# Kernel optimization log

Hardware: AMD Instinct MI355X
Metric: run time of the kernel (lower is better)

Reference implementation:

```python
import jax, jax.numpy as jnp
import numpy as np

B, S, D, V = 256, 128, 768, 30522
MASK_ID = 103
# vocab ids of the label words (8 positive, 6 neutral, 7 negative)
LABEL_IDS = [
    [2307, 2204, 3835, 2157, 6581, 2986, 5151, 3893],
    [7929, 24791, 8699, 4257, 16021, 6623],
    [6659, 2919, 11771, 3532, 11325, 4997, 13135],
]


def setup_inputs() -> dict:
    key = jax.random.key(0)
    ks = jax.random.split(key, 12)
    length = jax.random.randint(ks[0], (B,), 5, 105)          # 3+length <= 108 < S
    input_ids = jax.random.randint(ks[1], (B, S), 200, 30000)  # never hits MASK_ID
    input_ids = input_ids.at[jnp.arange(B), 3 + length].set(MASK_ID)  # one [MASK] per row
    bert_out = jax.random.normal(ks[2], (B, S, D), dtype=jnp.float32)
    p = lambda k, shp: 0.02 * jax.random.normal(k, shp, dtype=jnp.float32)
    return {
        'bert_out': bert_out,
        'input_ids': input_ids,
        'length': length,
        'senti_w': p(ks[3], (2, D)), 'senti_b': p(ks[4], (2,)),
        'dense_w': p(ks[5], (D, 2 * D)), 'dense_b': p(ks[6], (D,)),
        'dec_w': p(ks[7], (V, D)), 'dec_b': p(ks[8], (V,)),
        'w0': p(ks[9], (2, 8)), 'w1': p(ks[10], (2, 6)), 'w2': p(ks[11], (2, 7)),
    }


def reference(bert_out, input_ids, length, senti_w, senti_b, dense_w, dense_b,
              dec_w, dec_b, w0, w1, w2):
    # pooler -> sentiment head (Dropout is identity at inference)
    pooler = bert_out[:, 0]                                   # [B, D]
    category_out = pooler @ senti_w.T + senti_b               # [B, 2]

    # per-row [MASK] hidden state (exactly one MASK_ID per row)
    mask_pos = jnp.argmax(input_ids == MASK_ID, axis=1)       # [B]
    mask_logits = jnp.take_along_axis(bert_out, mask_pos[:, None, None], axis=1)[:, 0]  # [B, D]

    # attention(): softmax over the ragged slice bert_out[i, 3:3+length[i]]
    scores_raw = jnp.einsum('bsd,bd->bs', bert_out, mask_logits)        # [B, S]
    idx = jnp.arange(S)
    valid = (idx[None, :] >= 3) & (idx[None, :] < 3 + length[:, None])  # [B, S]
    scores = jax.nn.softmax(jnp.where(valid, scores_raw, -jnp.inf), axis=1)
    scores = jnp.where(valid, scores, 0.0)
    att = jnp.einsum('bs,bsd->bd', scores, bert_out)          # [B, D]

    feats = jnp.concatenate([att, mask_logits], axis=1)       # [B, 2D]
    h = jnp.tanh(feats @ dense_w.T + dense_b)                 # [B, D]
    probs = jnp.tanh(h @ dec_w.T + dec_b)                     # [B, V]

    outs = []
    for ids, w in zip(LABEL_IDS, (w0, w1, w2)):
        lp = probs[:, jnp.array(ids)]                         # [B, k]
        outs.append(lp @ w.T)                                 # [B, 2]
    out = jnp.stack(outs, axis=2)                             # [B, 2, 3]
    return category_out, out
```

## Files before the change

kernel.cpp:

```cpp
#include <hip/hip_runtime.h>
#include <hip/hip_bf16.h>
#include <math.h>

#define BB 256
#define SS 128
#define DD 768
#define K2 1536
#define MASK_ID 103

typedef __attribute__((ext_vector_type(8))) short short8;
typedef __attribute__((ext_vector_type(4))) float floatx4;

__constant__ int c_ids[21] = {
    2307, 2204, 3835, 2157, 6581, 2986, 5151, 3893,
    7929, 24791, 8699, 4257, 16021, 6623,
    6659, 2919, 11771, 3532, 11325, 4997, 13135
};

__device__ __forceinline__ float waveReduceSum(float v) {
    #pragma unroll
    for (int off = 32; off > 0; off >>= 1) v += __shfl_down(v, off, 64);
    return v;
}
__device__ __forceinline__ unsigned short f2bf(float f) {
    unsigned int u = __float_as_uint(f);
    u += 0x7FFF + ((u >> 16) & 1);
    return (unsigned short)(u >> 16);
}

__global__ __launch_bounds__(1024) void k_att(
    const float* __restrict__ bert, const int* __restrict__ ids,
    const int* __restrict__ len, const float* __restrict__ senti_w,
    const float* __restrict__ senti_b, float* __restrict__ cat_out,
    unsigned short* __restrict__ feats,
    const float* __restrict__ dense_w, unsigned short* __restrict__ dwb)
{
    __shared__ __align__(16) float s_mask[DD];
    __shared__ __align__(16) float s_part[16][DD];
    __shared__ float s_m[16], s_l[16], s_scale[16];
    __shared__ float s_red[32];
    __shared__ float s_M;
    __shared__ int s_mp;

    const int b = blockIdx.x;
    const int tid = threadIdx.x;
    const int lane = tid & 63;
    const int wave = tid >> 6;

    if (tid == 0) s_mp = SS;

    {
        const int n4 = DD * K2 / 4;
        for (int i = b * 1024 + tid; i < n4; i += BB * 1024) {
            float4 v = ((const float4*)dense_w)[i];
            ushort4 o;
            o.x = f2bf(v.x); o.y = f2bf(v.y); o.z = f2bf(v.z); o.w = f2bf(v.w);
            ((ushort4*)dwb)[i] = o;
        }
    }

    __syncthreads();
    if (tid < SS && ids[b * SS + tid] == MASK_ID) atomicMin(&s_mp, tid);
    __syncthreads();
    const int mp = (s_mp == SS) ? 0 : s_mp;
    const int L = len[b];
    const float* base = bert + (size_t)b * SS * DD;
    const float* mrow = base + (size_t)mp * DD;

    float c0 = 0.f, c1 = 0.f;
    if (tid < DD) {
        s_mask[tid] = mrow[tid];
        float x = base[tid];
        c0 = x * senti_w[tid];
        c1 = x * senti_w[DD + tid];
    }
    c0 = waveReduceSum(c0);
    c1 = waveReduceSum(c1);
    if (lane == 0) { s_red[wave] = c0; s_red[16 + wave] = c1; }
    __syncthreads();
    if (tid == 0) {
        float t0 = 0.f, t1 = 0.f;
        #pragma unroll
        for (int w = 0; w < 16; ++w) { t0 += s_red[w]; t1 += s_red[16 + w]; }
        cat_out[b * 2 + 0] = t0 + senti_b[0];
        cat_out[b * 2 + 1] = t1 + senti_b[1];
    }

    const float4* m4 = (const float4*)s_mask;
    float4 mm0 = m4[lane], mm1 = m4[lane + 64], mm2 = m4[lane + 128];
    float4 A0 = {0,0,0,0}, A1 = {0,0,0,0}, A2 = {0,0,0,0};
    float mloc = -INFINITY, lloc = 0.f;
    const int end = 3 + L;
    int s = 3 + wave;
    for (; s + 48 < end; s += 64) {
        const float4* r0 = (const float4*)(base + (size_t)s * DD);
        const float4* r1 = (const float4*)(base + (size_t)(s + 16) * DD);
        const float4* r2 = (const float4*)(base + (size_t)(s + 32) * DD);
        const float4* r3 = (const float4*)(base + (size_t)(s + 48) * DD);
        float4 a0 = r0[lane], a1 = r0[lane + 64], a2 = r0[lane + 128];
        float4 b0 = r1[lane], b1 = r1[lane + 64], b2 = r1[lane + 128];
        float4 c0v = r2[lane], c1v = r2[lane + 64], c2v = r2[lane + 128];
        float4 e0 = r3[lane], e1 = r3[lane + 64], e2 = r3[lane + 128];
        float d1 = a0.x*mm0.x + a0.y*mm0.y + a0.z*mm0.z + a0.w*mm0.w
                 + a1.x*mm1.x + a1.y*mm1.y + a1.z*mm1.z + a1.w*mm1.w
                 + a2.x*mm2.x + a2.y*mm2.y + a2.z*mm2.z + a2.w*mm2.w;
        float d2 = b0.x*mm0.x + b0.y*mm0.y + b0.z*mm0.z + b0.w*mm0.w
                 + b1.x*mm1.x + b1.y*mm1.y + b1.z*mm1.z + b1.w*mm1.w
                 + b2.x*mm2.x + b2.y*mm2.y + b2.z*mm2.z + b2.w*mm2.w;
        float d3 = c0v.x*mm0.x + c0v.y*mm0.y + c0v.z*mm0.z + c0v.w*mm0.w
                 + c1v.x*mm1.x + c1v.y*mm1.y + c1v.z*mm1.z + c1v.w*mm1.w
                 + c2v.x*mm2.x + c2v.y*mm2.y + c2v.z*mm2.z + c2v.w*mm2.w;
        float d4 = e0.x*mm0.x + e0.y*mm0.y + e0.z*mm0.z + e0.w*mm0.w
                 + e1.x*mm1.x + e1.y*mm1.y + e1.z*mm1.z + e1.w*mm1.w
                 + e2.x*mm2.x + e2.y*mm2.y + e2.z*mm2.z + e2.w*mm2.w;
        #pragma unroll
        for (int off = 32; off > 0; off >>= 1) {
            d1 += __shfl_xor(d1, off, 64);
            d2 += __shfl_xor(d2, off, 64);
            d3 += __shfl_xor(d3, off, 64);
            d4 += __shfl_xor(d4, off, 64);
        }
        float mnew = fmaxf(fmaxf(fmaxf(d1, d2), fmaxf(d3, d4)), mloc);
        float scale = __expf(mloc - mnew);
        float p1 = __expf(d1 - mnew);
        float p2 = __expf(d2 - mnew);
        float p3 = __expf(d3 - mnew);
        float p4 = __expf(d4 - mnew);
        lloc = lloc * scale + p1 + p2 + p3 + p4;
        A0.x = A0.x*scale + p1*a0.x + p2*b0.x + p3*c0v.x + p4*e0.x;
        A0.y = A0.y*scale + p1*a0.y + p2*b0.y + p3*c0v.y + p4*e0.y;
        A0.z = A0.z*scale + p1*a0.z + p2*b0.z + p3*c0v.z + p4*e0.z;
        A0.w = A0.w*scale + p1*a0.w + p2*b0.w + p3*c0v.w + p4*e0.w;
        A1.x = A1.x*scale + p1*a1.x + p2*b1.x + p3*c1v.x + p4*e1.x;
        A1.y = A1.y*scale + p1*a1.y + p2*b1.y + p3*c1v.y + p4*e1.y;
        A1.z = A1.z*scale + p1*a1.z + p2*b1.z + p3*c1v.z + p4*e1.z;
        A1.w = A1.w*scale + p1*a1.w + p2*b1.w + p3*c1v.w + p4*e1.w;
        A2.x = A2.x*scale + p1*a2.x + p2*b2.x + p3*c2v.x + p4*e2.x;
        A2.y = A2.y*scale + p1*a2.y + p2*b2.y + p3*c2v.y + p4*e2.y;
        A2.z = A2.z*scale + p1*a2.z + p2*b2.z + p3*c2v.z + p4*e2.z;
        A2.w = A2.w*scale + p1*a2.w + p2*b2.w + p3*c2v.w + p4*e2.w;
        mloc = mnew;
    }
    for (; s + 16 < end; s += 32) {
        const float4* ra = (const float4*)(base + (size_t)s * DD);
        const float4* rb = (const float4*)(base + (size_t)(s + 16) * DD);
        float4 a0 = ra[lane], a1 = ra[lane + 64], a2 = ra[lane + 128];
        float4 b0 = rb[lane], b1 = rb[lane + 64], b2 = rb[lane + 128];
        float d1 = a0.x*mm0.x + a0.y*mm0.y + a0.z*mm0.z + a0.w*mm0.w
                 + a1.x*mm1.x + a1.y*mm1.y + a1.z*mm1.z + a1.w*mm1.w
                 + a2.x*mm2.x + a2.y*mm2.y + a2.z*mm2.z + a2.w*mm2.w;
        float d2 = b0.x*mm0.x + b0.y*mm0.y + b0.z*mm0.z + b0.w*mm0.w
                 + b1.x*mm1.x + b1.y*mm1.y + b1.z*mm1.z + b1.w*mm1.w
                 + b2.x*mm2.x + b2.y*mm2.y + b2.z*mm2.z + b2.w*mm2.w;
        #pragma unroll
        for (int off = 32; off > 0; off >>= 1) {
            d1 += __shfl_xor(d1, off, 64);
            d2 += __shfl_xor(d2, off, 64);
        }
        float mnew = fmaxf(mloc, fmaxf(d1, d2));
        float scale = __expf(mloc - mnew);
        float p1 = __expf(d1 - mnew);
        float p2 = __expf(d2 - mnew);
        lloc = lloc * scale + p1 + p2;
        A0.x = A0.x*scale + p1*a0.x + p2*b0.x; A0.y = A0.y*scale + p1*a0.y + p2*b0.y;
        A0.z = A0.z*scale + p1*a0.z + p2*b0.z; A0.w = A0.w*scale + p1*a0.w + p2*b0.w;
        A1.x = A1.x*scale + p1*a1.x + p2*b1.x; A1.y = A1.y*scale + p1*a1.y + p2*b1.y;
        A1.z = A1.z*scale + p1*a1.z + p2*b1.z; A1.w = A1.w*scale + p1*a1.w + p2*b1.w;
        A2.x = A2.x*scale + p1*a2.x + p2*b2.x; A2.y = A2.y*scale + p1*a2.y + p2*b2.y;
        A2.z = A2.z*scale + p1*a2.z + p2*b2.z; A2.w = A2.w*scale + p1*a2.w + p2*b2.w;
        mloc = mnew;
    }
    for (; s < end; s += 16) {
        const float4* ra = (const float4*)(base + (size_t)s * DD);
        float4 a0 = ra[lane], a1 = ra[lane + 64], a2 = ra[lane + 128];
        float d1 = a0.x*mm0.x + a0.y*mm0.y + a0.z*mm0.z + a0.w*mm0.w
                 + a1.x*mm1.x + a1.y*mm1.y + a1.z*mm1.z + a1.w*mm1.w
                 + a2.x*mm2.x + a2.y*mm2.y + a2.z*mm2.z + a2.w*mm2.w;
        #pragma unroll
        for (int off = 32; off > 0; off >>= 1) d1 += __shfl_xor(d1, off, 64);
        float mnew = fmaxf(mloc, d1);
        float scale = __expf(mloc - mnew);
        float p1 = __expf(d1 - mnew);
        lloc = lloc * scale + p1;
        A0.x = A0.x*scale + p1*a0.x; A0.y = A0.y*scale + p1*a0.y;
        A0.z = A0.z*scale + p1*a0.z; A0.w = A0.w*scale + p1*a0.w;
        A1.x = A1.x*scale + p1*a1.x; A1.y = A1.y*scale + p1*a1.y;
        A1.z = A1.z*scale + p1*a1.z; A1.w = A1.w*scale + p1*a1.w;
        A2.x = A2.x*scale + p1*a2.x; A2.y = A2.y*scale + p1*a2.y;
        A2.z = A2.z*scale + p1*a2.z; A2.w = A2.w*scale + p1*a2.w;
        mloc = mnew;
    }
    if (lane == 0) { s_m[wave] = mloc; s_l[wave] = lloc; }
    float4* pw = (float4*)s_part[wave];
    pw[lane] = A0; pw[lane + 64] = A1; pw[lane + 128] = A2;
    __syncthreads();

    if (tid == 0) {
        float M = -INFINITY;
        #pragma unroll
        for (int w = 0; w < 16; ++w) M = fmaxf(M, s_m[w]);
        s_M = M;
    }
    __syncthreads();
    if (tid < 16) s_scale[tid] = __expf(s_m[tid] - s_M);
    __syncthreads();

    if (tid < DD) {
        float lt = 0.f, a = 0.f;
        #pragma unroll
        for (int w = 0; w < 16; ++w) {
            lt += s_scale[w] * s_l[w];
            a  += s_scale[w] * s_part[w][tid];
        }
        unsigned short* fb = feats + (size_t)b * K2;
        fb[tid]      = f2bf(a / lt);
        fb[DD + tid] = f2bf(s_mask[tid]);
    }
}

__global__ __launch_bounds__(512) void k_dense(
    const unsigned short* __restrict__ featsb,
    const unsigned short* __restrict__ dwb,
    const float* __restrict__ db, float* __restrict__ h)
{
    __shared__ floatx4 s_acc[4][64];
    const int tid = threadIdx.x;
    const int lane = tid & 63, wave = tid >> 6;
    const int wq = wave & 3, kh = wave >> 2;
    const int b0 = blockIdx.y * 32 + (wq >> 1) * 16;
    const int j0 = blockIdx.x * 32 + (wq & 1) * 16;
    const int m = lane & 15, q = lane >> 4;

    const short8* Arow = (const short8*)(featsb + (size_t)(b0 + m) * K2) + kh * 96;
    const short8* Brow = (const short8*)(dwb + (size_t)(j0 + m) * K2) + kh * 96;
    floatx4 acc = {0.f, 0.f, 0.f, 0.f};
    #pragma unroll 6
    for (int k8 = 0; k8 < 96; k8 += 4) {
        short8 a = Arow[k8 + q];
        short8 w = Brow[k8 + q];
        acc = __builtin_amdgcn_mfma_f32_16x16x32_bf16(a, w, acc, 0, 0, 0);
    }
    if (kh) s_acc[wq][lane] = acc;
    __syncthreads();
    if (!kh) {
        floatx4 o = s_acc[wq][lane];
        acc.x += o.x; acc.y += o.y; acc.z += o.z; acc.w += o.w;
        const int col = j0 + m;
        const int rb = b0 + q * 4;
        const float bias = db[col];
        #pragma unroll
        for (int r = 0; r < 4; ++r)
            h[(size_t)(rb + r) * DD + col] = tanhf(acc[r] + bias);
    }
}

__global__ __launch_bounds__(256) void k_dec(
    const float* __restrict__ h, const float* __restrict__ dec_w,
    const float* __restrict__ dec_b, const float* __restrict__ w0,
    const float* __restrict__ w1, const float* __restrict__ w2,
    float* __restrict__ out)
{
    __shared__ __align__(16) float s_h[DD];
    __shared__ float s_p[21];
    const int b = blockIdx.x;
    const int tid = threadIdx.x;
    const int lane = tid & 63, wave = tid >> 6;

    for (int d = tid; d < DD; d += 256) s_h[d] = h[(size_t)b * DD + d];
    __syncthreads();

    const float4* h4 = (const float4*)s_h;
    float4 x0 = h4[lane], x1 = h4[lane + 64], x2 = h4[lane + 128];

    for (int idx = wave; idx < 21; idx += 4) {
        const int vid = c_ids[idx];
        const float4* wr = (const float4*)(dec_w + (size_t)vid * DD);
        float4 v0 = wr[lane], v1 = wr[lane + 64], v2 = wr[lane + 128];
        float acc = x0.x*v0.x + x0.y*v0.y + x0.z*v0.z + x0.w*v0.w
                  + x1.x*v1.x + x1.y*v1.y + x1.z*v1.z + x1.w*v1.w
                  + x2.x*v2.x + x2.y*v2.y + x2.z*v2.z + x2.w*v2.w;
        acc = waveReduceSum(acc);
        if (lane == 0) s_p[idx] = tanhf(acc + dec_b[vid]);
    }
    __syncthreads();

    if (tid < 6) {
        const int c = tid / 3, g = tid % 3;
        const float* wg = (g == 0) ? w0 : (g == 1) ? w1 : w2;
        const int n    = (g == 0) ? 8  : (g == 1) ? 6  : 7;
        const int base = (g == 0) ? 0  : (g == 1) ? 8  : 14;
        float acc = 0.f;
        for (int i = 0; i < n; ++i) acc += s_p[base + i] * wg[c * n + i];
        out[(size_t)b * 6 + c * 3 + g] = acc;
    }
}

extern "C" void kernel_launch(void* const* d_in, const int* in_sizes, int n_in,
                              void* d_out, int out_size, void* d_ws, size_t ws_size,
                              hipStream_t stream) {
    const float* bert    = (const float*)d_in[0];
    const int*   ids     = (const int*)  d_in[1];
    const int*   len     = (const int*)  d_in[2];
    const float* senti_w = (const float*)d_in[3];
    const float* senti_b = (const float*)d_in[4];
    const float* dense_w = (const float*)d_in[5];
    const float* dense_b = (const float*)d_in[6];
    const float* dec_w   = (const float*)d_in[7];
    const float* dec_b   = (const float*)d_in[8];
    const float* w0      = (const float*)d_in[9];
    const float* w1      = (const float*)d_in[10];
    const float* w2      = (const float*)d_in[11];
    float* out = (float*)d_out;

    unsigned short* feats = (unsigned short*)d_ws;
    unsigned short* dwb   = feats + (size_t)BB * K2;
    float* h = (float*)(dwb + (size_t)DD * K2);

    k_att<<<BB, 1024, 0, stream>>>(bert, ids, len, senti_w, senti_b, out,
                                   feats, dense_w, dwb);
    k_dense<<<dim3(24, 8), 512, 0, stream>>>(feats, dwb, dense_b, h);
    k_dec<<<BB, 256, 0, stream>>>(h, dec_w, dec_b, w0, w1, w2, out + BB * 2);
}
```

Measured before the change: 221.4 us.

## Fuse dense projection and label-word decoder into one kernel via shared memory

Merges the dense bf16 MFMA GEMM and the label-word decoder/projection into a single kernel. Each 1024-thread block handles 16 batch rows and keeps the tanh hidden states in LDS instead of writing them to global memory. This removes one kernel launch and the global round trip of h. In exchange, the GEMM runs on only 16 blocks with longer per-wave K loops, which reduces parallelism across the GPU.

```diff
diff --git a/kernel.cpp b/kernel.cpp
--- a/kernel.cpp
+++ b/kernel.cpp
@@ -218,80 +218,72 @@
     }
 }
 
-__global__ __launch_bounds__(512) void k_dense(
+#define HP 772
+__global__ __launch_bounds__(1024) void k_dd(
     const unsigned short* __restrict__ featsb,
     const unsigned short* __restrict__ dwb,
-    const float* __restrict__ db, float* __restrict__ h)
+    const float* __restrict__ db,
+    const float* __restrict__ dec_w, const float* __restrict__ dec_b,
+    const float* __restrict__ w0, const float* __restrict__ w1,
+    const float* __restrict__ w2, float* __restrict__ out)
 {
-    __shared__ floatx4 s_acc[4][64];
+    __shared__ __align__(16) float s_h[16][HP];
+    __shared__ float s_p[16][21];
     const int tid = threadIdx.x;
     const int lane = tid & 63, wave = tid >> 6;
-    const int wq = wave & 3, kh = wave >> 2;
-    const int b0 = blockIdx.y * 32 + (wq >> 1) * 16;
-    const int j0 = blockIdx.x * 32 + (wq & 1) * 16;
+    const int b0 = blockIdx.x * 16;
     const int m = lane & 15, q = lane >> 4;
 
-    const short8* Arow = (const short8*)(featsb + (size_t)(b0 + m) * K2) + kh * 96;
-    const short8* Brow = (const short8*)(dwb + (size_t)(j0 + m) * K2) + kh * 96;
-    floatx4 acc = {0.f, 0.f, 0.f, 0.f};
-    #pragma unroll 6
-    for (int k8 = 0; k8 < 96; k8 += 4) {
+    const int j0 = wave * 48;
+    const short8* Arow = (const short8*)(featsb + (size_t)(b0 + m) * K2);
+    const short8* B0 = (const short8*)(dwb + (size_t)(j0      + m) * K2);
+    const short8* B1 = (const short8*)(dwb + (size_t)(j0 + 16 + m) * K2);
+    const short8* B2 = (const short8*)(dwb + (size_t)(j0 + 32 + m) * K2);
+    floatx4 ac0 = {0,0,0,0}, ac1 = {0,0,0,0}, ac2 = {0,0,0,0};
+    #pragma unroll 2
+    for (int k8 = 0; k8 < 192; k8 += 4) {
         short8 a = Arow[k8 + q];
-        short8 w = Brow[k8 + q];
-        acc = __builtin_amdgcn_mfma_f32_16x16x32_bf16(a, w, acc, 0, 0, 0);
-    }
-    if (kh) s_acc[wq][lane] = acc;
-    __syncthreads();
-    if (!kh) {
-        floatx4 o = s_acc[wq][lane];
-        acc.x += o.x; acc.y += o.y; acc.z += o.z; acc.w += o.w;
-        const int col = j0 + m;
-        const int rb = b0 + q * 4;
-        const float bias = db[col];
-        #pragma unroll
-        for (int r = 0; r < 4; ++r)
-            h[(size_t)(rb + r) * DD + col] = tanhf(acc[r] + bias);
-    }
-}
-
-__global__ __launch_bounds__(256) void k_dec(
-    const float* __restrict__ h, const float* __restrict__ dec_w,
-    const float* __restrict__ dec_b, const float* __restrict__ w0,
-    const float* __restrict__ w1, const float* __restrict__ w2,
-    float* __restrict__ out)
-{
-    __shared__ __align__(16) float s_h[DD];
-    __shared__ float s_p[21];
-    const int b = blockIdx.x;
-    const int tid = threadIdx.x;
-    const int lane = tid & 63, wave = tid >> 6;
-
-    for (int d = tid; d < DD; d += 256) s_h[d] = h[(size_t)b * DD + d];
-    __syncthreads();
-
-    const float4* h4 = (const float4*)s_h;
-    float4 x0 = h4[lane], x1 = h4[lane + 64], x2 = h4[lane + 128];
-
-    for (int idx = wave; idx < 21; idx += 4) {
-        const int vid = c_ids[idx];
-        const float4* wr = (const float4*)(dec_w + (size_t)vid * DD);
-        float4 v0 = wr[lane], v1 = wr[lane + 64], v2 = wr[lane + 128];
-        float acc = x0.x*v0.x + x0.y*v0.y + x0.z*v0.z + x0.w*v0.w
-                  + x1.x*v1.x + x1.y*v1.y + x1.z*v1.z + x1.w*v1.w
-                  + x2.x*v2.x + x2.y*v2.y + x2.z*v2.z + x2.w*v2.w;
-        acc = waveReduceSum(acc);
-        if (lane == 0) s_p[idx] = tanhf(acc + dec_b[vid]);
-    }
-    __syncthreads();
-
-    if (tid < 6) {
-        const int c = tid / 3, g = tid % 3;
+        ac0 = __builtin_amdgcn_mfma_f32_16x16x32_bf16(a, B0[k8 + q], ac0, 0, 0, 0);
+        ac1 = __builtin_amdgcn_mfma_f32_16x16x32_bf16(a, B1[k8 + q], ac1, 0, 0, 0);
+        ac2 = __builtin_amdgcn_mfma_f32_16x16x32_bf16(a, B2[k8 + q], ac2, 0, 0, 0);
+    }
+    {
+        const int rb = q * 4;
+        const float d0 = db[j0 + m], d1 = db[j0 + 16 + m], d2 = db[j0 + 32 + m];
+        #pragma unroll
+        for (int r = 0; r < 4; ++r) {
+            s_h[rb + r][j0 + m]      = tanhf(ac0[r] + d0);
+            s_h[rb + r][j0 + 16 + m] = tanhf(ac1[r] + d1);
+            s_h[rb + r][j0 + 32 + m] = tanhf(ac2[r] + d2);
+        }
+    }
+    __syncthreads();
+
+    {
+        const float4* h4 = (const float4*)s_h[wave];
+        float4 x0 = h4[lane], x1 = h4[lane + 64], x2 = h4[lane + 128];
+        for (int v = 0; v < 21; ++v) {
+            const int vid = c_ids[v];
+            const float4* wr = (const float4*)(dec_w + (size_t)vid * DD);
+            float4 v0 = wr[lane], v1 = wr[lane + 64], v2 = wr[lane + 128];
+            float acc = x0.x*v0.x + x0.y*v0.y + x0.z*v0.z + x0.w*v0.w
+                      + x1.x*v1.x + x1.y*v1.y + x1.z*v1.z + x1.w*v1.w
+                      + x2.x*v2.x + x2.y*v2.y + x2.z*v2.z + x2.w*v2.w;
+            acc = waveReduceSum(acc);
+            if (lane == 0) s_p[wave][v] = tanhf(acc + dec_b[vid]);
+        }
+    }
+    __syncthreads();
+
+    if (tid < 96) {
+        const int bi = tid / 6, r6 = tid % 6;
+        const int c = r6 / 3, g = r6 % 3;
         const float* wg = (g == 0) ? w0 : (g == 1) ? w1 : w2;
         const int n    = (g == 0) ? 8  : (g == 1) ? 6  : 7;
         const int base = (g == 0) ? 0  : (g == 1) ? 8  : 14;
         float acc = 0.f;
-        for (int i = 0; i < n; ++i) acc += s_p[base + i] * wg[c * n + i];
-        out[(size_t)b * 6 + c * 3 + g] = acc;
+        for (int i = 0; i < n; ++i) acc += s_p[bi][base + i] * wg[c * n + i];
+        out[(size_t)(b0 + bi) * 6 + c * 3 + g] = acc;
     }
 }
 
@@ -314,10 +306,9 @@
 
     unsigned short* feats = (unsigned short*)d_ws;
     unsigned short* dwb   = feats + (size_t)BB * K2;
-    float* h = (float*)(dwb + (size_t)DD * K2);
 
     k_att<<<BB, 1024, 0, stream>>>(bert, ids, len, senti_w, senti_b, out,
                                    feats, dense_w, dwb);
-    k_dense<<<dim3(24, 8), 512, 0, stream>>>(feats, dwb, dense_b, h);
-    k_dec<<<BB, 256, 0, stream>>>(h, dec_w, dec_b, w0, w1, w2, out + BB * 2);
-}
+    k_dd<<<16, 1024, 0, stream>>>(feats, dwb, dense_b, dec_w, dec_b,
+                                  w0, w1, w2, out + BB * 2);
+}
```

Measured after the change: 308.0 us. 1.39x slower.
